# Performance work log

Measured on AMD Instinct MI355X. Metric: run time of the kernel, lower is better.

Reference implementation:

```python
import jax, jax.numpy as jnp
import numpy as np

B, S, H, A = 64, 2048, 512, 512


def setup_inputs() -> dict:
    key = jax.random.key(0)
    k1, k2, k3, k4, k5 = jax.random.split(key, 5)
    nn_outs = jax.random.normal(k1, (B, S, H), dtype=jnp.float32)
    # lengths in [1, S] so every row has at least one valid step
    batch_lens = jax.random.randint(k2, (B,), 1, S + 1, dtype=jnp.int64)
    # learned params: context vector ~ U(-0.1, 0.1), Linear(H -> A)
    context = jax.random.uniform(k3, (A,), dtype=jnp.float32, minval=-0.1, maxval=0.1)
    proj_w = jax.random.uniform(k4, (A, H), dtype=jnp.float32, minval=-0.1, maxval=0.1)
    proj_b = jax.random.uniform(k5, (A,), dtype=jnp.float32, minval=-0.1, maxval=0.1)
    return {"nn_outs": nn_outs, "batch_lens": batch_lens,
            "context": context, "proj_w": proj_w, "proj_b": proj_b}


def reference(nn_outs, batch_lens, context, proj_w, proj_b):
    # proj = tanh(Linear(nn_outs)): (B, S, A)
    proj = jnp.tanh(jnp.einsum('bsh,ah->bsa', nn_outs, proj_w) + proj_b)
    # attention scores: (B, S)
    scores = jnp.einsum('bsa,a->bs', proj, context)
    # variable-length masked softmax (replaces the per-batch python loop)
    mask = jnp.arange(nn_outs.shape[1])[None, :] < batch_lens[:, None]  # (B, S)
    scores = jnp.where(mask, scores, -jnp.inf)
    atten = jax.nn.softmax(scores, axis=-1)
    atten = jnp.where(mask, atten, 0.0)  # padded positions exactly zero
    # weighted sum over steps: (B, H)
    return jnp.einsum('bs,bsh->bh', atten, nn_outs)
```

## Files before the change

kernel.cpp:

```cpp
#include <hip/hip_runtime.h>

#define BB 64
#define SS 2048
#define HH 512
#define MROWS (BB*SS)

typedef __attribute__((ext_vector_type(8))) short short8;
typedef __attribute__((ext_vector_type(4))) float f32x4;

__device__ inline unsigned short f2bf(float f){
  unsigned int u = __float_as_uint(f);
  u += 0x7FFFu + ((u >> 16) & 1u);
  return (unsigned short)(u >> 16);
}

__device__ inline int read_len(const void* lens, int i){
  const int* p = (const int*)lens;
  if (p[1] == 0) return (int)((const long long*)lens)[i];
  return p[i];
}

__device__ inline float fast_tanh(float x){
  x = fminf(fmaxf(x, -15.f), 15.f);
  float e = __expf(2.f * x);
  return (e - 1.f) / (e + 1.f);
}

__device__ inline void gload16(const void* gptr, void* lptr){
  __builtin_amdgcn_global_load_lds(
      (const __attribute__((address_space(1))) void*)gptr,
      (__attribute__((address_space(3))) void*)lptr, 16, 0, 0);
}

__device__ inline short8 cvt8p(float4 x0, float4 x1){
  short8 r;
  r[0] = (short)f2bf(x0.x); r[1] = (short)f2bf(x0.y);
  r[2] = (short)f2bf(x0.z); r[3] = (short)f2bf(x0.w);
  r[4] = (short)f2bf(x1.x); r[5] = (short)f2bf(x1.y);
  r[6] = (short)f2bf(x1.z); r[7] = (short)f2bf(x1.w);
  return r;
}

__global__ __launch_bounds__(256) void convw_kernel(
    const float* __restrict__ W, unsigned short* __restrict__ Wb)
{
  size_t base = (size_t)blockIdx.x * 64 * HH;
  int t = threadIdx.x;
  #pragma unroll
  for (int j = 0; j < 32; j++) {
    size_t idx = base + (size_t)j * 1024 + t * 4;
    float4 v = *(const float4*)(W + idx);
    unsigned int p0 = (unsigned int)f2bf(v.x) | ((unsigned int)f2bf(v.y) << 16);
    unsigned int p1 = (unsigned int)f2bf(v.z) | ((unsigned int)f2bf(v.w) << 16);
    *(uint2*)(Wb + idx) = make_uint2(p0, p1);
  }
}

__global__ __launch_bounds__(512, 2) void scores_n512(
    const float* __restrict__ X, const unsigned short* __restrict__ Wb,
    const void* __restrict__ lens, const float* __restrict__ ctx,
    const float* __restrict__ pb, float* __restrict__ scr)
{
  int bid = blockIdx.x;
  int mtile = (bid & 7) * 128 + (bid >> 3);
  int s_start = (mtile * 128) & (SS - 1);
  int b = (mtile * 128) >> 11;
  if (s_start >= read_len(lens, b)) return;

  __shared__ __align__(16) unsigned short As[128 * 64];
  __shared__ __align__(16) unsigned short Bs[2][512 * 64];

  int tid = threadIdx.x;
  int lane = tid & 63;
  int w = tid >> 6;
  int wm = w >> 2, wn = w & 3;
  int l15 = lane & 15, g = lane >> 4;

  f32x4 acc[4][8];
  #pragma unroll
  for (int i = 0; i < 4; i++)
    #pragma unroll
    for (int j = 0; j < 8; j++) acc[i][j] = (f32x4)0.f;

  int arow = tid >> 2;
  int alg0 = (tid & 3) * 2;
  const float* Ag = X + (size_t)(mtile * 128 + arow) * HH + alg0 * 8;
  int apg0 = (alg0)     ^ (arow & 7);
  int apg1 = (alg0 + 1) ^ (arow & 7);

  int brow = lane >> 3;
  int blg = (lane & 7) ^ brow;
  const unsigned short* Bg = Wb + (size_t)brow * HH + blg * 8;

  float4 ar[4];

#define A_ISSUE(KT) { const float* p_ = Ag + (KT); \
    ar[0] = *(const float4*)p_;       ar[1] = *(const float4*)(p_ + 4); \
    ar[2] = *(const float4*)(p_ + 8); ar[3] = *(const float4*)(p_ + 12); }

#define A_WRITE() { \
    *(short8*)&As[arow * 64 + apg0 * 8] = cvt8p(ar[0], ar[1]); \
    *(short8*)&As[arow * 64 + apg1 * 8] = cvt8p(ar[2], ar[3]); }

#define B_ISSUE(BUF, KT) { _Pragma("unroll") for (int i_ = 0; i_ < 8; i_++) { \
    int j_ = w * 8 + i_; \
    gload16(Bg + (size_t)(j_ * 8) * HH + (KT), &Bs[BUF][(j_ * 8) * 64]); } }

  A_ISSUE(0)
  B_ISSUE(0, 0)
  A_WRITE()
  __syncthreads();

  int cur = 0;
  for (int t = 0; t < 8; ++t) {
    if (t < 7) {
      A_ISSUE((t + 1) * 64)
      B_ISSUE(cur ^ 1, (t + 1) * 64)
    }
    #pragma unroll
    for (int kk = 0; kk < 64; kk += 32) {
      int ga = g + (kk >> 3);
      int pga = (ga ^ (l15 & 7)) * 8;
      short8 af[4];
      #pragma unroll
      for (int im = 0; im < 4; im++) {
        int r = wm * 64 + im * 16 + l15;
        af[im] = *(const short8*)&As[r * 64 + pga];
      }
      #pragma unroll
      for (int in = 0; in < 8; in++) {
        int r2 = wn * 128 + in * 16 + l15;
        short8 bfr = *(const short8*)&Bs[cur][r2 * 64 + pga];
        #pragma unroll
        for (int im = 0; im < 4; im++)
          acc[im][in] = __builtin_amdgcn_mfma_f32_16x16x32_bf16(
              af[im], bfr, acc[im][in], 0, 0, 0);
      }
    }
    __syncthreads();
    if (t < 7) A_WRITE()
    __syncthreads();
    cur ^= 1;
  }

  float pbv[8], ctxv[8];
  #pragma unroll
  for (int in = 0; in < 8; in++) {
    int a_g = wn * 128 + in * 16 + l15;
    pbv[in] = pb[a_g];
    ctxv[in] = ctx[a_g];
  }
  float* red = (float*)As;
  #pragma unroll
  for (int im = 0; im < 4; im++) {
    #pragma unroll
    for (int r = 0; r < 4; r++) {
      float rowsum = 0.f;
      #pragma unroll
      for (int in = 0; in < 8; in++)
        rowsum += fast_tanh(acc[im][in][r] + pbv[in]) * ctxv[in];
      #pragma unroll
      for (int m = 1; m < 16; m <<= 1)
        rowsum += __shfl_xor(rowsum, m, 64);
      if (l15 == 0)
        red[wn * 128 + wm * 64 + im * 16 + g * 4 + r] = rowsum;
    }
  }
  __syncthreads();
  if (tid < 128) {
    float s = red[tid] + red[128 + tid] + red[256 + tid] + red[384 + tid];
    scr[(size_t)mtile * 128 + tid] = s;
  }
}

__global__ __launch_bounds__(256) void softmax_kernel(
    const float* __restrict__ scr, const void* __restrict__ lens,
    float* __restrict__ wts)
{
  int b = blockIdx.x;
  int tid = threadIdx.x;
  int len = read_len(lens, b);
  float sc[8];
  #pragma unroll
  for (int i = 0; i < 8; i++)
    sc[i] = scr[(size_t)b * SS + tid + i * 256];
  float m = -1e30f;
  #pragma unroll
  for (int i = 0; i < 8; i++)
    if (tid + i * 256 < len) m = fmaxf(m, sc[i]);
  #pragma unroll
  for (int off = 1; off < 64; off <<= 1) m = fmaxf(m, __shfl_xor(m, off, 64));
  __shared__ float redm[4];
  __shared__ float reds[4];
  int w = tid >> 6, lane = tid & 63;
  if (lane == 0) redm[w] = m;
  __syncthreads();
  m = fmaxf(fmaxf(redm[0], redm[1]), fmaxf(redm[2], redm[3]));
  float e[8]; float sum = 0.f;
  #pragma unroll
  for (int i = 0; i < 8; i++) {
    int s = tid + i * 256;
    e[i] = (s < len) ? __expf(sc[i] - m) : 0.f;
    sum += e[i];
  }
  #pragma unroll
  for (int off = 1; off < 64; off <<= 1) sum += __shfl_xor(sum, off, 64);
  if (lane == 0) reds[w] = sum;
  __syncthreads();
  sum = reds[0] + reds[1] + reds[2] + reds[3];
  float inv = 1.f / sum;
  #pragma unroll
  for (int i = 0; i < 8; i++) {
    int s = tid + i * 256;
    wts[(size_t)b * SS + s] = e[i] * inv;
  }
}

__global__ __launch_bounds__(256) void softmax8_kernel(
    const float* __restrict__ sp, const void* __restrict__ lens,
    float* __restrict__ wts)
{
  int b = blockIdx.x;
  int tid = threadIdx.x;
  int len = read_len(lens, b);
  float sc[8];
  #pragma unroll
  for (int i = 0; i < 8; i++) {
    int s = tid + i * 256;
    size_t row = (size_t)b * SS + s;
    float v = 0.f;
    #pragma unroll
    for (int p = 0; p < 8; p++) v += sp[(size_t)p * MROWS + row];
    sc[i] = v;
  }
  float m = -1e30f;
  #pragma unroll
  for (int i = 0; i < 8; i++)
    if (tid + i * 256 < len) m = fmaxf(m, sc[i]);
  #pragma unroll
  for (int off = 1; off < 64; off <<= 1) m = fmaxf(m, __shfl_xor(m, off, 64));
  __shared__ float redm[4];
  __shared__ float reds[4];
  int w = tid >> 6, lane = tid & 63;
  if (lane == 0) redm[w] = m;
  __syncthreads();
  m = fmaxf(fmaxf(redm[0], redm[1]), fmaxf(redm[2], redm[3]));
  float e[8]; float sum = 0.f;
  #pragma unroll
  for (int i = 0; i < 8; i++) {
    int s = tid + i * 256;
    e[i] = (s < len) ? __expf(sc[i] - m) : 0.f;
    sum += e[i];
  }
  #pragma unroll
  for (int off = 1; off < 64; off <<= 1) sum += __shfl_xor(sum, off, 64);
  if (lane == 0) reds[w] = sum;
  __syncthreads();
  sum = reds[0] + reds[1] + reds[2] + reds[3];
  float inv = 1.f / sum;
  #pragma unroll
  for (int i = 0; i < 8; i++) {
    int s = tid + i * 256;
    wts[(size_t)b * SS + s] = e[i] * inv;
  }
}

__global__ __launch_bounds__(256) void wsum_kernel(
    const float* __restrict__ X, const float* __restrict__ wts,
    const void* __restrict__ lens, float* __restrict__ op)
{
  int sc = blockIdx.x;
  int b  = blockIdx.y;
  int tid = threadIdx.x;
  int s0 = sc * 128;
  int len = read_len(lens, b);
  int cnt = min(128, len - s0);
  float* o = op + ((size_t)sc * BB + b) * HH;
  if (cnt <= 0) {
    *(float2*)(o + tid * 2) = make_float2(0.f, 0.f);
    return;
  }
  __shared__ float wsh[128];
  __shared__ f32x4 red[128];
  if (tid < 128) wsh[tid] = wts[(size_t)b * SS + s0 + tid];
  __syncthreads();
  int h = (tid & 127) * 4;
  int sr = tid >> 7;
  f32x4 acc = (f32x4)0.f;
  for (int i = sr; i < cnt; i += 2) {
    float wv = wsh[i];
    const float* xr = X + ((size_t)b * SS + s0 + i) * HH + h;
    float4 xv = *(const float4*)xr;
    acc[0] += wv * xv.x;
    acc[1] += wv * xv.y;
    acc[2] += wv * xv.z;
    acc[3] += wv * xv.w;
  }
  if (sr == 1) red[tid & 127] = acc;
  __syncthreads();
  if (sr == 0) {
    f32x4 r2 = red[tid];
    acc[0] += r2[0]; acc[1] += r2[1]; acc[2] += r2[2]; acc[3] += r2[3];
    *(f32x4*)(o + h) = acc;
  }
}

__global__ __launch_bounds__(512) void reduce_kernel(
    const float* __restrict__ op, float* __restrict__ out)
{
  int b = blockIdx.x;
  int h = threadIdx.x;
  float v = 0.f;
  #pragma unroll
  for (int sc = 0; sc < 16; sc++) v += op[((size_t)sc * BB + b) * HH + h];
  out[(size_t)b * HH + h] = v;
}

__global__ __launch_bounds__(256) void scores_fb(
    const float* __restrict__ X, const void* __restrict__ lens,
    const float* __restrict__ ctx, const float* __restrict__ W,
    const float* __restrict__ pb, float* __restrict__ sp)
{
  int bid = blockIdx.x;
  int wg = (bid & 7) * 512 + (bid >> 3);
  int ntile = wg & 3;
  int mtile = wg >> 2;
  int s_start = (mtile * 128) & (SS - 1);
  int b = (mtile * 128) >> 11;
  if (s_start >= read_len(lens, b)) return;

  __shared__ unsigned short As[128 * 72];
  __shared__ unsigned short Bs[128 * 72];

  int tid = threadIdx.x;
  int lane = tid & 63;
  int w = tid >> 6;
  int wm = w >> 1, wn = w & 1;
  int l15 = lane & 15, g = lane >> 4;

  f32x4 acc[4][4];
  #pragma unroll
  for (int i = 0; i < 4; i++)
    #pragma unroll
    for (int j = 0; j < 4; j++) acc[i][j] = (f32x4)0.f;

  int srow = tid >> 4;
  int scol = (tid & 15) * 4;
  const float* Xbase = X + (size_t)(mtile * 128) * HH;
  const float* Wbase = W + (size_t)(ntile * 128) * HH;

  for (int kt = 0; kt < HH; kt += 64) {
    #pragma unroll
    for (int i = 0; i < 8; i++) {
      int row = srow + i * 16;
      float4 va = *(const float4*)(Xbase + (size_t)row * HH + kt + scol);
      unsigned int p0 = (unsigned int)f2bf(va.x) | ((unsigned int)f2bf(va.y) << 16);
      unsigned int p1 = (unsigned int)f2bf(va.z) | ((unsigned int)f2bf(va.w) << 16);
      *(uint2*)&As[row * 72 + scol] = make_uint2(p0, p1);
      float4 vb = *(const float4*)(Wbase + (size_t)row * HH + kt + scol);
      unsigned int q0 = (unsigned int)f2bf(vb.x) | ((unsigned int)f2bf(vb.y) << 16);
      unsigned int q1 = (unsigned int)f2bf(vb.z) | ((unsigned int)f2bf(vb.w) << 16);
      *(uint2*)&Bs[row * 72 + scol] = make_uint2(q0, q1);
    }
    __syncthreads();
    #pragma unroll
    for (int kk = 0; kk < 64; kk += 32) {
      short8 af[4], bfr[4];
      int ko = kk + g * 8;
      #pragma unroll
      for (int im = 0; im < 4; im++)
        af[im] = *(const short8*)&As[(wm * 64 + im * 16 + l15) * 72 + ko];
      #pragma unroll
      for (int in = 0; in < 4; in++)
        bfr[in] = *(const short8*)&Bs[(wn * 64 + in * 16 + l15) * 72 + ko];
      #pragma unroll
      for (int im = 0; im < 4; im++)
        #pragma unroll
        for (int in = 0; in < 4; in++)
          acc[im][in] = __builtin_amdgcn_mfma_f32_16x16x32_bf16(
              af[im], bfr[in], acc[im][in], 0, 0, 0);
    }
    __syncthreads();
  }

  #pragma unroll
  for (int im = 0; im < 4; im++) {
    #pragma unroll
    for (int r = 0; r < 4; r++) {
      float rowsum = 0.f;
      #pragma unroll
      for (int in = 0; in < 4; in++) {
        int a_g = ntile * 128 + wn * 64 + in * 16 + l15;
        rowsum += fast_tanh(acc[im][in][r] + pb[a_g]) * ctx[a_g];
      }
      #pragma unroll
      for (int m = 1; m < 16; m <<= 1)
        rowsum += __shfl_xor(rowsum, m, 64);
      if (l15 == 0) {
        int rowg = mtile * 128 + wm * 64 + im * 16 + g * 4 + r;
        sp[(size_t)(ntile * 2 + wn) * MROWS + rowg] = rowsum;
      }
    }
  }
}

extern "C" void kernel_launch(void* const* d_in, const int* in_sizes, int n_in,
                              void* d_out, int out_size, void* d_ws, size_t ws_size,
                              hipStream_t stream) {
  const float* X   = (const float*)d_in[0];
  const void*  lens = d_in[1];
  const float* ctx = (const float*)d_in[2];
  const float* W   = (const float*)d_in[3];
  const float* pb  = (const float*)d_in[4];
  float* out = (float*)d_out;

  char* ws = (char*)d_ws;
  const size_t WB_BYTES = (size_t)HH * HH * 2;
  const size_t SC_BYTES = (size_t)MROWS * 4;
  const size_t WT_BYTES = (size_t)BB * SS * 4;
  const size_t OP_BYTES = 16ull * BB * HH * 4;
  const size_t NEED = WB_BYTES + SC_BYTES + WT_BYTES + OP_BYTES;

  if (ws_size >= NEED) {
    unsigned short* Wb = (unsigned short*)ws;
    float* scr = (float*)(ws + WB_BYTES);
    float* wts = (float*)(ws + WB_BYTES + SC_BYTES);
    float* op  = (float*)(ws + WB_BYTES + SC_BYTES + WT_BYTES);

    convw_kernel<<<8, 256, 0, stream>>>(W, Wb);
    scores_n512<<<1024, 512, 0, stream>>>(X, Wb, lens, ctx, pb, scr);
    softmax_kernel<<<BB, 256, 0, stream>>>(scr, lens, wts);
    wsum_kernel<<<dim3(16, BB), 256, 0, stream>>>(X, wts, lens, op);
    reduce_kernel<<<BB, 512, 0, stream>>>(op, out);
  } else {
    const size_t SP_BYTES = 8ull * MROWS * 4;
    float* sp  = (float*)ws;
    float* wts = (float*)(ws + SP_BYTES);
    float* op  = (float*)(ws + SP_BYTES + WT_BYTES);

    scores_fb<<<4096, 256, 0, stream>>>(X, lens, ctx, W, pb, sp);
    softmax8_kernel<<<BB, 256, 0, stream>>>(sp, lens, wts);
    wsum_kernel<<<dim3(16, BB), 256, 0, stream>>>(X, wts, lens, op);
    reduce_kernel<<<BB, 512, 0, stream>>>(op, out);
  }
}
```

Baseline: 131.4 us.

## Restructure scores GEMM to 1024-thread blocks with padded K=32 double buffers

The scores kernel is rewritten to use 16 waves per block (2x8 wave grid, 4x4 MFMA tiles per wave) instead of 8 waves with 4x8 tiles. The K step drops from 64 to 32, and both A and B are double-buffered in LDS using padded rows of stride 40 rather than XOR swizzling. B is now loaded through registers instead of direct global-to-LDS loads, and the blockIdx remapping is removed. Per-wave register pressure falls and the loop needs one barrier per iteration instead of two, at the cost of twice as many iterations and a different LDS bank-conflict pattern.

```diff
diff --git a/kernel.cpp b/kernel.cpp
--- a/kernel.cpp
+++ b/kernel.cpp
@@ -26,19 +26,10 @@
   return (e - 1.f) / (e + 1.f);
 }
 
-__device__ inline void gload16(const void* gptr, void* lptr){
-  __builtin_amdgcn_global_load_lds(
-      (const __attribute__((address_space(1))) void*)gptr,
-      (__attribute__((address_space(3))) void*)lptr, 16, 0, 0);
-}
-
-__device__ inline short8 cvt8p(float4 x0, float4 x1){
-  short8 r;
-  r[0] = (short)f2bf(x0.x); r[1] = (short)f2bf(x0.y);
-  r[2] = (short)f2bf(x0.z); r[3] = (short)f2bf(x0.w);
-  r[4] = (short)f2bf(x1.x); r[5] = (short)f2bf(x1.y);
-  r[6] = (short)f2bf(x1.z); r[7] = (short)f2bf(x1.w);
-  return r;
+__device__ inline uint2 cvt4p(float4 v){
+  unsigned int p0 = (unsigned int)f2bf(v.x) | ((unsigned int)f2bf(v.y) << 16);
+  unsigned int p1 = (unsigned int)f2bf(v.z) | ((unsigned int)f2bf(v.w) << 16);
+  return make_uint2(p0, p1);
 }
 
 __global__ __launch_bounds__(256) void convw_kernel(
@@ -50,103 +41,87 @@
   for (int j = 0; j < 32; j++) {
     size_t idx = base + (size_t)j * 1024 + t * 4;
     float4 v = *(const float4*)(W + idx);
-    unsigned int p0 = (unsigned int)f2bf(v.x) | ((unsigned int)f2bf(v.y) << 16);
-    unsigned int p1 = (unsigned int)f2bf(v.z) | ((unsigned int)f2bf(v.w) << 16);
-    *(uint2*)(Wb + idx) = make_uint2(p0, p1);
-  }
-}
-
-__global__ __launch_bounds__(512, 2) void scores_n512(
+    *(uint2*)(Wb + idx) = cvt4p(v);
+  }
+}
+
+__global__ __launch_bounds__(1024) void scores_v10(
     const float* __restrict__ X, const unsigned short* __restrict__ Wb,
     const void* __restrict__ lens, const float* __restrict__ ctx,
     const float* __restrict__ pb, float* __restrict__ scr)
 {
-  int bid = blockIdx.x;
-  int mtile = (bid & 7) * 128 + (bid >> 3);
+  int mtile = blockIdx.x;
   int s_start = (mtile * 128) & (SS - 1);
   int b = (mtile * 128) >> 11;
   if (s_start >= read_len(lens, b)) return;
 
-  __shared__ __align__(16) unsigned short As[128 * 64];
-  __shared__ __align__(16) unsigned short Bs[2][512 * 64];
+  __shared__ __align__(16) unsigned short As[2][128 * 40];
+  __shared__ __align__(16) unsigned short Bs[2][512 * 40];
 
   int tid = threadIdx.x;
   int lane = tid & 63;
   int w = tid >> 6;
-  int wm = w >> 2, wn = w & 3;
+  int wm = w >> 3, wn = w & 7;
   int l15 = lane & 15, g = lane >> 4;
 
-  f32x4 acc[4][8];
+  f32x4 acc[4][4];
   #pragma unroll
   for (int i = 0; i < 4; i++)
     #pragma unroll
-    for (int j = 0; j < 8; j++) acc[i][j] = (f32x4)0.f;
-
-  int arow = tid >> 2;
-  int alg0 = (tid & 3) * 2;
-  const float* Ag = X + (size_t)(mtile * 128 + arow) * HH + alg0 * 8;
-  int apg0 = (alg0)     ^ (arow & 7);
-  int apg1 = (alg0 + 1) ^ (arow & 7);
-
-  int brow = lane >> 3;
-  int blg = (lane & 7) ^ brow;
-  const unsigned short* Bg = Wb + (size_t)brow * HH + blg * 8;
-
-  float4 ar[4];
-
-#define A_ISSUE(KT) { const float* p_ = Ag + (KT); \
-    ar[0] = *(const float4*)p_;       ar[1] = *(const float4*)(p_ + 4); \
-    ar[2] = *(const float4*)(p_ + 8); ar[3] = *(const float4*)(p_ + 12); }
-
-#define A_WRITE() { \
-    *(short8*)&As[arow * 64 + apg0 * 8] = cvt8p(ar[0], ar[1]); \
-    *(short8*)&As[arow * 64 + apg1 * 8] = cvt8p(ar[2], ar[3]); }
-
-#define B_ISSUE(BUF, KT) { _Pragma("unroll") for (int i_ = 0; i_ < 8; i_++) { \
-    int j_ = w * 8 + i_; \
-    gload16(Bg + (size_t)(j_ * 8) * HH + (KT), &Bs[BUF][(j_ * 8) * 64]); } }
-
-  A_ISSUE(0)
-  B_ISSUE(0, 0)
-  A_WRITE()
+    for (int j = 0; j < 4; j++) acc[i][j] = (f32x4)0.f;
+
+  int arow = tid >> 3;
+  int acg  = tid & 7;
+  const float* Ag = X + (size_t)(mtile * 128 + arow) * HH + acg * 4;
+
+  int brow = tid >> 1;
+  int bh   = tid & 1;
+  const unsigned short* Bg = Wb + (size_t)brow * HH + bh * 16;
+
+  float4 av;
+  short8 bv0, bv1;
+
+#define ISSUE(KT) { \
+    av  = *(const float4*)(Ag + (KT)); \
+    bv0 = *(const short8*)(Bg + (KT)); \
+    bv1 = *(const short8*)(Bg + (KT) + 8); }
+
+#define WRITE(BUF) { \
+    *(uint2*)&As[BUF][arow * 40 + acg * 4] = cvt4p(av); \
+    *(short8*)&Bs[BUF][brow * 40 + bh * 16]     = bv0; \
+    *(short8*)&Bs[BUF][brow * 40 + bh * 16 + 8] = bv1; }
+
+  ISSUE(0)
+  WRITE(0)
   __syncthreads();
 
   int cur = 0;
-  for (int t = 0; t < 8; ++t) {
-    if (t < 7) {
-      A_ISSUE((t + 1) * 64)
-      B_ISSUE(cur ^ 1, (t + 1) * 64)
-    }
-    #pragma unroll
-    for (int kk = 0; kk < 64; kk += 32) {
-      int ga = g + (kk >> 3);
-      int pga = (ga ^ (l15 & 7)) * 8;
-      short8 af[4];
-      #pragma unroll
-      for (int im = 0; im < 4; im++) {
-        int r = wm * 64 + im * 16 + l15;
-        af[im] = *(const short8*)&As[r * 64 + pga];
-      }
-      #pragma unroll
-      for (int in = 0; in < 8; in++) {
-        int r2 = wn * 128 + in * 16 + l15;
-        short8 bfr = *(const short8*)&Bs[cur][r2 * 64 + pga];
-        #pragma unroll
-        for (int im = 0; im < 4; im++)
-          acc[im][in] = __builtin_amdgcn_mfma_f32_16x16x32_bf16(
-              af[im], bfr, acc[im][in], 0, 0, 0);
-      }
-    }
-    __syncthreads();
-    if (t < 7) A_WRITE()
+  for (int t = 0; t < 16; ++t) {
+    if (t < 15) ISSUE((t + 1) * 32)
+    short8 af[4];
+    #pragma unroll
+    for (int im = 0; im < 4; im++) {
+      int r = wm * 64 + im * 16 + l15;
+      af[im] = *(const short8*)&As[cur][r * 40 + g * 8];
+    }
+    #pragma unroll
+    for (int in = 0; in < 4; in++) {
+      int r2 = wn * 64 + in * 16 + l15;
+      short8 bfr = *(const short8*)&Bs[cur][r2 * 40 + g * 8];
+      #pragma unroll
+      for (int im = 0; im < 4; im++)
+        acc[im][in] = __builtin_amdgcn_mfma_f32_16x16x32_bf16(
+            af[im], bfr, acc[im][in], 0, 0, 0);
+    }
+    if (t < 15) WRITE(cur ^ 1)
     __syncthreads();
     cur ^= 1;
   }
 
-  float pbv[8], ctxv[8];
-  #pragma unroll
-  for (int in = 0; in < 8; in++) {
-    int a_g = wn * 128 + in * 16 + l15;
+  float pbv[4], ctxv[4];
+  #pragma unroll
+  for (int in = 0; in < 4; in++) {
+    int a_g = wn * 64 + in * 16 + l15;
     pbv[in] = pb[a_g];
     ctxv[in] = ctx[a_g];
   }
@@ -157,18 +132,22 @@
     for (int r = 0; r < 4; r++) {
       float rowsum = 0.f;
       #pragma unroll
-      for (int in = 0; in < 8; in++)
+      for (int in = 0; in < 4; in++)
         rowsum += fast_tanh(acc[im][in][r] + pbv[in]) * ctxv[in];
       #pragma unroll
       for (int m = 1; m < 16; m <<= 1)
         rowsum += __shfl_xor(rowsum, m, 64);
-      if (l15 == 0)
-        red[wn * 128 + wm * 64 + im * 16 + g * 4 + r] = rowsum;
+      if (l15 == 0) {
+        int rowg = wm * 64 + im * 16 + g * 4 + r;
+        red[wn * 128 + rowg] = rowsum;
+      }
     }
   }
   __syncthreads();
   if (tid < 128) {
-    float s = red[tid] + red[128 + tid] + red[256 + tid] + red[384 + tid];
+    float s = 0.f;
+    #pragma unroll
+    for (int q = 0; q < 8; q++) s += red[q * 128 + tid];
     scr[(size_t)mtile * 128 + tid] = s;
   }
 }
@@ -184,55 +163,6 @@
   #pragma unroll
   for (int i = 0; i < 8; i++)
     sc[i] = scr[(size_t)b * SS + tid + i * 256];
-  float m = -1e30f;
-  #pragma unroll
-  for (int i = 0; i < 8; i++)
-    if (tid + i * 256 < len) m = fmaxf(m, sc[i]);
-  #pragma unroll
-  for (int off = 1; off < 64; off <<= 1) m = fmaxf(m, __shfl_xor(m, off, 64));
-  __shared__ float redm[4];
-  __shared__ float reds[4];
-  int w = tid >> 6, lane = tid & 63;
-  if (lane == 0) redm[w] = m;
-  __syncthreads();
-  m = fmaxf(fmaxf(redm[0], redm[1]), fmaxf(redm[2], redm[3]));
-  float e[8]; float sum = 0.f;
-  #pragma unroll
-  for (int i = 0; i < 8; i++) {
-    int s = tid + i * 256;
-    e[i] = (s < len) ? __expf(sc[i] - m) : 0.f;
-    sum += e[i];
-  }
-  #pragma unroll
-  for (int off = 1; off < 64; off <<= 1) sum += __shfl_xor(sum, off, 64);
-  if (lane == 0) reds[w] = sum;
-  __syncthreads();
-  sum = reds[0] + reds[1] + reds[2] + reds[3];
-  float inv = 1.f / sum;
-  #pragma unroll
-  for (int i = 0; i < 8; i++) {
-    int s = tid + i * 256;
-    wts[(size_t)b * SS + s] = e[i] * inv;
-  }
-}
-
-__global__ __launch_bounds__(256) void softmax8_kernel(
-    const float* __restrict__ sp, const void* __restrict__ lens,
-    float* __restrict__ wts)
-{
-  int b = blockIdx.x;
-  int tid = threadIdx.x;
-  int len = read_len(lens, b);
-  float sc[8];
-  #pragma unroll
-  for (int i = 0; i < 8; i++) {
-    int s = tid + i * 256;
-    size_t row = (size_t)b * SS + s;
-    float v = 0.f;
-    #pragma unroll
-    for (int p = 0; p < 8; p++) v += sp[(size_t)p * MROWS + row];
-    sc[i] = v;
-  }
   float m = -1e30f;
   #pragma unroll
   for (int i = 0; i < 8; i++)
@@ -354,13 +284,9 @@
     for (int i = 0; i < 8; i++) {
       int row = srow + i * 16;
       float4 va = *(const float4*)(Xbase + (size_t)row * HH + kt + scol);
-      unsigned int p0 = (unsigned int)f2bf(va.x) | ((unsigned int)f2bf(va.y) << 16);
-      unsigned int p1 = (unsigned int)f2bf(va.z) | ((unsigned int)f2bf(va.w) << 16);
-      *(uint2*)&As[row * 72 + scol] = make_uint2(p0, p1);
+      *(uint2*)&As[row * 72 + scol] = cvt4p(va);
       float4 vb = *(const float4*)(Wbase + (size_t)row * HH + kt + scol);
-      unsigned int q0 = (unsigned int)f2bf(vb.x) | ((unsigned int)f2bf(vb.y) << 16);
-      unsigned int q1 = (unsigned int)f2bf(vb.z) | ((unsigned int)f2bf(vb.w) << 16);
-      *(uint2*)&Bs[row * 72 + scol] = make_uint2(q0, q1);
+      *(uint2*)&Bs[row * 72 + scol] = cvt4p(vb);
     }
     __syncthreads();
     #pragma unroll
@@ -401,6 +327,55 @@
         sp[(size_t)(ntile * 2 + wn) * MROWS + rowg] = rowsum;
       }
     }
+  }
+}
+
+__global__ __launch_bounds__(256) void softmax8_kernel(
+    const float* __restrict__ sp, const void* __restrict__ lens,
+    float* __restrict__ wts)
+{
+  int b = blockIdx.x;
+  int tid = threadIdx.x;
+  int len = read_len(lens, b);
+  float sc[8];
+  #pragma unroll
+  for (int i = 0; i < 8; i++) {
+    int s = tid + i * 256;
+    size_t row = (size_t)b * SS + s;
+    float v = 0.f;
+    #pragma unroll
+    for (int p = 0; p < 8; p++) v += sp[(size_t)p * MROWS + row];
+    sc[i] = v;
+  }
+  float m = -1e30f;
+  #pragma unroll
+  for (int i = 0; i < 8; i++)
+    if (tid + i * 256 < len) m = fmaxf(m, sc[i]);
+  #pragma unroll
+  for (int off = 1; off < 64; off <<= 1) m = fmaxf(m, __shfl_xor(m, off, 64));
+  __shared__ float redm[4];
+  __shared__ float reds[4];
+  int w = tid >> 6, lane = tid & 63;
+  if (lane == 0) redm[w] = m;
+  __syncthreads();
+  m = fmaxf(fmaxf(redm[0], redm[1]), fmaxf(redm[2], redm[3]));
+  float e[8]; float sum = 0.f;
+  #pragma unroll
+  for (int i = 0; i < 8; i++) {
+    int s = tid + i * 256;
+    e[i] = (s < len) ? __expf(sc[i] - m) : 0.f;
+    sum += e[i];
+  }
+  #pragma unroll
+  for (int off = 1; off < 64; off <<= 1) sum += __shfl_xor(sum, off, 64);
+  if (lane == 0) reds[w] = sum;
+  __syncthreads();
+  sum = reds[0] + reds[1] + reds[2] + reds[3];
+  float inv = 1.f / sum;
+  #pragma unroll
+  for (int i = 0; i < 8; i++) {
+    int s = tid + i * 256;
+    wts[(size_t)b * SS + s] = e[i] * inv;
   }
 }
 
@@ -428,7 +403,7 @@
     float* op  = (float*)(ws + WB_BYTES + SC_BYTES + WT_BYTES);
 
     convw_kernel<<<8, 256, 0, stream>>>(W, Wb);
-    scores_n512<<<1024, 512, 0, stream>>>(X, Wb, lens, ctx, pb, scr);
+    scores_v10<<<1024, 1024, 0, stream>>>(X, Wb, lens, ctx, pb, scr);
     softmax_kernel<<<BB, 256, 0, stream>>>(scr, lens, wts);
     wsum_kernel<<<dim3(16, BB), 256, 0, stream>>>(X, wts, lens, op);
     reduce_kernel<<<BB, 512, 0, stream>>>(op, out);
```

Measured after the change: 172.1 us. 1.31x slower.

## Double-buffer A tile in scores GEMM and fuse softmax into weighted-sum kernel

Applied to the files above, without the earlier changes.

The scores GEMM now double-buffers the bf16 A tile in shared memory, which removes one __syncthreads per k-step. Shared memory per block grows by 16 KB, which may affect occupancy at 2 blocks per CU. The separate softmax kernel is removed: each weighted-sum block recomputes the per-batch max and sum from the raw scores, then normalizes its own 128-step chunk. This drops one launch and the weights buffer round-trip, but every one of the 16 chunk blocks redundantly reads the full 2048-score row.

```diff
diff --git a/kernel.cpp b/kernel.cpp
--- a/kernel.cpp
+++ b/kernel.cpp
@@ -56,7 +56,7 @@
   }
 }
 
-__global__ __launch_bounds__(512, 2) void scores_n512(
+__global__ __launch_bounds__(512, 2) void scores_v11(
     const float* __restrict__ X, const unsigned short* __restrict__ Wb,
     const void* __restrict__ lens, const float* __restrict__ ctx,
     const float* __restrict__ pb, float* __restrict__ scr)
@@ -67,7 +67,7 @@
   int b = (mtile * 128) >> 11;
   if (s_start >= read_len(lens, b)) return;
 
-  __shared__ __align__(16) unsigned short As[128 * 64];
+  __shared__ __align__(16) unsigned short As[2][128 * 64];
   __shared__ __align__(16) unsigned short Bs[2][512 * 64];
 
   int tid = threadIdx.x;
@@ -98,9 +98,9 @@
     ar[0] = *(const float4*)p_;       ar[1] = *(const float4*)(p_ + 4); \
     ar[2] = *(const float4*)(p_ + 8); ar[3] = *(const float4*)(p_ + 12); }
 
-#define A_WRITE() { \
-    *(short8*)&As[arow * 64 + apg0 * 8] = cvt8p(ar[0], ar[1]); \
-    *(short8*)&As[arow * 64 + apg1 * 8] = cvt8p(ar[2], ar[3]); }
+#define A_WRITE(BUF) { \
+    *(short8*)&As[BUF][arow * 64 + apg0 * 8] = cvt8p(ar[0], ar[1]); \
+    *(short8*)&As[BUF][arow * 64 + apg1 * 8] = cvt8p(ar[2], ar[3]); }
 
 #define B_ISSUE(BUF, KT) { _Pragma("unroll") for (int i_ = 0; i_ < 8; i_++) { \
     int j_ = w * 8 + i_; \
@@ -108,7 +108,7 @@
 
   A_ISSUE(0)
   B_ISSUE(0, 0)
-  A_WRITE()
+  A_WRITE(0)
   __syncthreads();
 
   int cur = 0;
@@ -125,7 +125,7 @@
       #pragma unroll
       for (int im = 0; im < 4; im++) {
         int r = wm * 64 + im * 16 + l15;
-        af[im] = *(const short8*)&As[r * 64 + pga];
+        af[im] = *(const short8*)&As[cur][r * 64 + pga];
       }
       #pragma unroll
       for (int in = 0; in < 8; in++) {
@@ -137,8 +137,7 @@
               af[im], bfr, acc[im][in], 0, 0, 0);
       }
     }
-    __syncthreads();
-    if (t < 7) A_WRITE()
+    if (t < 7) A_WRITE(cur ^ 1)
     __syncthreads();
     cur ^= 1;
   }
@@ -173,8 +172,180 @@
   }
 }
 
-__global__ __launch_bounds__(256) void softmax_kernel(
-    const float* __restrict__ scr, const void* __restrict__ lens,
+__global__ __launch_bounds__(256) void wsum2_kernel(
+    const float* __restrict__ X, const float* __restrict__ scr,
+    const void* __restrict__ lens, float* __restrict__ op)
+{
+  int sc = blockIdx.x;
+  int b  = blockIdx.y;
+  int tid = threadIdx.x;
+  int s0 = sc * 128;
+  int len = read_len(lens, b);
+  int cnt = min(128, len - s0);
+  float* o = op + ((size_t)sc * BB + b) * HH;
+  if (cnt <= 0) {
+    *(float2*)(o + tid * 2) = make_float2(0.f, 0.f);
+    return;
+  }
+
+  __shared__ float redm[4], reds[4];
+  __shared__ float wsh[128];
+  __shared__ f32x4 red[128];
+
+  int wv = tid >> 6, lane = tid & 63;
+  float scv[8];
+  float m = -1e30f;
+  #pragma unroll
+  for (int i = 0; i < 8; i++) {
+    int s = tid + i * 256;
+    scv[i] = scr[(size_t)b * SS + s];
+    if (s < len) m = fmaxf(m, scv[i]);
+  }
+  #pragma unroll
+  for (int off = 1; off < 64; off <<= 1) m = fmaxf(m, __shfl_xor(m, off, 64));
+  if (lane == 0) redm[wv] = m;
+  __syncthreads();
+  m = fmaxf(fmaxf(redm[0], redm[1]), fmaxf(redm[2], redm[3]));
+  float sum = 0.f;
+  #pragma unroll
+  for (int i = 0; i < 8; i++) {
+    int s = tid + i * 256;
+    sum += (s < len) ? __expf(scv[i] - m) : 0.f;
+  }
+  #pragma unroll
+  for (int off = 1; off < 64; off <<= 1) sum += __shfl_xor(sum, off, 64);
+  if (lane == 0) reds[wv] = sum;
+  __syncthreads();
+  float inv = 1.f / (reds[0] + reds[1] + reds[2] + reds[3]);
+
+  if (tid < 128) {
+    int s = s0 + tid;
+    wsh[tid] = (s < len) ? __expf(scr[(size_t)b * SS + s] - m) * inv : 0.f;
+  }
+  __syncthreads();
+
+  int h = (tid & 127) * 4;
+  int sr = tid >> 7;
+  f32x4 acc = (f32x4)0.f;
+  for (int i = sr; i < cnt; i += 2) {
+    float wvv = wsh[i];
+    const float* xr = X + ((size_t)b * SS + s0 + i) * HH + h;
+    float4 xv = *(const float4*)xr;
+    acc[0] += wvv * xv.x;
+    acc[1] += wvv * xv.y;
+    acc[2] += wvv * xv.z;
+    acc[3] += wvv * xv.w;
+  }
+  if (sr == 1) red[tid & 127] = acc;
+  __syncthreads();
+  if (sr == 0) {
+    f32x4 r2 = red[tid];
+    acc[0] += r2[0]; acc[1] += r2[1]; acc[2] += r2[2]; acc[3] += r2[3];
+    *(f32x4*)(o + h) = acc;
+  }
+}
+
+__global__ __launch_bounds__(512) void reduce_kernel(
+    const float* __restrict__ op, float* __restrict__ out)
+{
+  int b = blockIdx.x;
+  int h = threadIdx.x;
+  float v = 0.f;
+  #pragma unroll
+  for (int sc = 0; sc < 16; sc++) v += op[((size_t)sc * BB + b) * HH + h];
+  out[(size_t)b * HH + h] = v;
+}
+
+__global__ __launch_bounds__(256) void scores_fb(
+    const float* __restrict__ X, const void* __restrict__ lens,
+    const float* __restrict__ ctx, const float* __restrict__ W,
+    const float* __restrict__ pb, float* __restrict__ sp)
+{
+  int bid = blockIdx.x;
+  int wg = (bid & 7) * 512 + (bid >> 3);
+  int ntile = wg & 3;
+  int mtile = wg >> 2;
+  int s_start = (mtile * 128) & (SS - 1);
+  int b = (mtile * 128) >> 11;
+  if (s_start >= read_len(lens, b)) return;
+
+  __shared__ unsigned short As[128 * 72];
+  __shared__ unsigned short Bs[128 * 72];
+
+  int tid = threadIdx.x;
+  int lane = tid & 63;
+  int w = tid >> 6;
+  int wm = w >> 1, wn = w & 1;
+  int l15 = lane & 15, g = lane >> 4;
+
+  f32x4 acc[4][4];
+  #pragma unroll
+  for (int i = 0; i < 4; i++)
+    #pragma unroll
+    for (int j = 0; j < 4; j++) acc[i][j] = (f32x4)0.f;
+
+  int srow = tid >> 4;
+  int scol = (tid & 15) * 4;
+  const float* Xbase = X + (size_t)(mtile * 128) * HH;
+  const float* Wbase = W + (size_t)(ntile * 128) * HH;
+
+  for (int kt = 0; kt < HH; kt += 64) {
+    #pragma unroll
+    for (int i = 0; i < 8; i++) {
+      int row = srow + i * 16;
+      float4 va = *(const float4*)(Xbase + (size_t)row * HH + kt + scol);
+      unsigned int p0 = (unsigned int)f2bf(va.x) | ((unsigned int)f2bf(va.y) << 16);
+      unsigned int p1 = (unsigned int)f2bf(va.z) | ((unsigned int)f2bf(va.w) << 16);
+      *(uint2*)&As[row * 72 + scol] = make_uint2(p0, p1);
+      float4 vb = *(const float4*)(Wbase + (size_t)row * HH + kt + scol);
+      unsigned int q0 = (unsigned int)f2bf(vb.x) | ((unsigned int)f2bf(vb.y) << 16);
+      unsigned int q1 = (unsigned int)f2bf(vb.z) | ((unsigned int)f2bf(vb.w) << 16);
+      *(uint2*)&Bs[row * 72 + scol] = make_uint2(q0, q1);
+    }
+    __syncthreads();
+    #pragma unroll
+    for (int kk = 0; kk < 64; kk += 32) {
+      short8 af[4], bfr[4];
+      int ko = kk + g * 8;
+      #pragma unroll
+      for (int im = 0; im < 4; im++)
+        af[im] = *(const short8*)&As[(wm * 64 + im * 16 + l15) * 72 + ko];
+      #pragma unroll
+      for (int in = 0; in < 4; in++)
+        bfr[in] = *(const short8*)&Bs[(wn * 64 + in * 16 + l15) * 72 + ko];
+      #pragma unroll
+      for (int im = 0; im < 4; im++)
+        #pragma unroll
+        for (int in = 0; in < 4; in++)
+          acc[im][in] = __builtin_amdgcn_mfma_f32_16x16x32_bf16(
+              af[im], bfr[in], acc[im][in], 0, 0, 0);
+    }
+    __syncthreads();
+  }
+
+  #pragma unroll
+  for (int im = 0; im < 4; im++) {
+    #pragma unroll
+    for (int r = 0; r < 4; r++) {
+      float rowsum = 0.f;
+      #pragma unroll
+      for (int in = 0; in < 4; in++) {
+        int a_g = ntile * 128 + wn * 64 + in * 16 + l15;
+        rowsum += fast_tanh(acc[im][in][r] + pb[a_g]) * ctx[a_g];
+      }
+      #pragma unroll
+      for (int m = 1; m < 16; m <<= 1)
+        rowsum += __shfl_xor(rowsum, m, 64);
+      if (l15 == 0) {
+        int rowg = mtile * 128 + wm * 64 + im * 16 + g * 4 + r;
+        sp[(size_t)(ntile * 2 + wn) * MROWS + rowg] = rowsum;
+      }
+    }
+  }
+}
+
+__global__ __launch_bounds__(256) void softmax8_kernel(
+    const float* __restrict__ sp, const void* __restrict__ lens,
     float* __restrict__ wts)
 {
   int b = blockIdx.x;
@@ -182,8 +353,14 @@
   int len = read_len(lens, b);
   float sc[8];
   #pragma unroll
-  for (int i = 0; i < 8; i++)
-    sc[i] = scr[(size_t)b * SS + tid + i * 256];
+  for (int i = 0; i < 8; i++) {
+    int s = tid + i * 256;
+    size_t row = (size_t)b * SS + s;
+    float v = 0.f;
+    #pragma unroll
+    for (int p = 0; p < 8; p++) v += sp[(size_t)p * MROWS + row];
+    sc[i] = v;
+  }
   float m = -1e30f;
   #pragma unroll
   for (int i = 0; i < 8; i++)
@@ -216,56 +393,7 @@
   }
 }
 
-__global__ __launch_bounds__(256) void softmax8_kernel(
-    const float* __restrict__ sp, const void* __restrict__ lens,
-    float* __restrict__ wts)
-{
-  int b = blockIdx.x;
-  int tid = threadIdx.x;
-  int len = read_len(lens, b);
-  float sc[8];
-  #pragma unroll
-  for (int i = 0; i < 8; i++) {
-    int s = tid + i * 256;
-    size_t row = (size_t)b * SS + s;
-    float v = 0.f;
-    #pragma unroll
-    for (int p = 0; p < 8; p++) v += sp[(size_t)p * MROWS + row];
-    sc[i] = v;
-  }
-  float m = -1e30f;
-  #pragma unroll
-  for (int i = 0; i < 8; i++)
-    if (tid + i * 256 < len) m = fmaxf(m, sc[i]);
-  #pragma unroll
-  for (int off = 1; off < 64; off <<= 1) m = fmaxf(m, __shfl_xor(m, off, 64));
-  __shared__ float redm[4];
-  __shared__ float reds[4];
-  int w = tid >> 6, lane = tid & 63;
-  if (lane == 0) redm[w] = m;
-  __syncthreads();
-  m = fmaxf(fmaxf(redm[0], redm[1]), fmaxf(redm[2], redm[3]));
-  float e[8]; float sum = 0.f;
-  #pragma unroll
-  for (int i = 0; i < 8; i++) {
-    int s = tid + i * 256;
-    e[i] = (s < len) ? __expf(sc[i] - m) : 0.f;
-    sum += e[i];
-  }
-  #pragma unroll
-  for (int off = 1; off < 64; off <<= 1) sum += __shfl_xor(sum, off, 64);
-  if (lane == 0) reds[w] = sum;
-  __syncthreads();
-  sum = reds[0] + reds[1] + reds[2] + reds[3];
-  float inv = 1.f / sum;
-  #pragma unroll
-  for (int i = 0; i < 8; i++) {
-    int s = tid + i * 256;
-    wts[(size_t)b * SS + s] = e[i] * inv;
-  }
-}
-
-__global__ __launch_bounds__(256) void wsum_kernel(
+__global__ __launch_bounds__(256) void wsum_fb(
     const float* __restrict__ X, const float* __restrict__ wts,
     const void* __restrict__ lens, float* __restrict__ op)
 {
@@ -305,105 +433,6 @@
   }
 }
 
-__global__ __launch_bounds__(512) void reduce_kernel(
-    const float* __restrict__ op, float* __restrict__ out)
-{
-  int b = blockIdx.x;
-  int h = threadIdx.x;
-  float v = 0.f;
-  #pragma unroll
-  for (int sc = 0; sc < 16; sc++) v += op[((size_t)sc * BB + b) * HH + h];
-  out[(size_t)b * HH + h] = v;
-}
-
-__global__ __launch_bounds__(256) void scores_fb(
-    const float* __restrict__ X, const void* __restrict__ lens,
-    const float* __restrict__ ctx, const float* __restrict__ W,
-    const float* __restrict__ pb, float* __restrict__ sp)
-{
-  int bid = blockIdx.x;
-  int wg = (bid & 7) * 512 + (bid >> 3);
-  int ntile = wg & 3;
-  int mtile = wg >> 2;
-  int s_start = (mtile * 128) & (SS - 1);
-  int b = (mtile * 128) >> 11;
-  if (s_start >= read_len(lens, b)) return;
-
-  __shared__ unsigned short As[128 * 72];
-  __shared__ unsigned short Bs[128 * 72];
-
-  int tid = threadIdx.x;
-  int lane = tid & 63;
-  int w = tid >> 6;
-  int wm = w >> 1, wn = w & 1;
-  int l15 = lane & 15, g = lane >> 4;
-
-  f32x4 acc[4][4];
-  #pragma unroll
-  for (int i = 0; i < 4; i++)
-    #pragma unroll
-    for (int j = 0; j < 4; j++) acc[i][j] = (f32x4)0.f;
-
-  int srow = tid >> 4;
-  int scol = (tid & 15) * 4;
-  const float* Xbase = X + (size_t)(mtile * 128) * HH;
-  const float* Wbase = W + (size_t)(ntile * 128) * HH;
-
-  for (int kt = 0; kt < HH; kt += 64) {
-    #pragma unroll
-    for (int i = 0; i < 8; i++) {
-      int row = srow + i * 16;
-      float4 va = *(const float4*)(Xbase + (size_t)row * HH + kt + scol);
-      unsigned int p0 = (unsigned int)f2bf(va.x) | ((unsigned int)f2bf(va.y) << 16);
-      unsigned int p1 = (unsigned int)f2bf(va.z) | ((unsigned int)f2bf(va.w) << 16);
-      *(uint2*)&As[row * 72 + scol] = make_uint2(p0, p1);
-      float4 vb = *(const float4*)(Wbase + (size_t)row * HH + kt + scol);
-      unsigned int q0 = (unsigned int)f2bf(vb.x) | ((unsigned int)f2bf(vb.y) << 16);
-      unsigned int q1 = (unsigned int)f2bf(vb.z) | ((unsigned int)f2bf(vb.w) << 16);
-      *(uint2*)&Bs[row * 72 + scol] = make_uint2(q0, q1);
-    }
-    __syncthreads();
-    #pragma unroll
-    for (int kk = 0; kk < 64; kk += 32) {
-      short8 af[4], bfr[4];
-      int ko = kk + g * 8;
-      #pragma unroll
-      for (int im = 0; im < 4; im++)
-        af[im] = *(const short8*)&As[(wm * 64 + im * 16 + l15) * 72 + ko];
-      #pragma unroll
-      for (int in = 0; in < 4; in++)
-        bfr[in] = *(const short8*)&Bs[(wn * 64 + in * 16 + l15) * 72 + ko];
-      #pragma unroll
-      for (int im = 0; im < 4; im++)
-        #pragma unroll
-        for (int in = 0; in < 4; in++)
-          acc[im][in] = __builtin_amdgcn_mfma_f32_16x16x32_bf16(
-              af[im], bfr[in], acc[im][in], 0, 0, 0);
-    }
-    __syncthreads();
-  }
-
-  #pragma unroll
-  for (int im = 0; im < 4; im++) {
-    #pragma unroll
-    for (int r = 0; r < 4; r++) {
-      float rowsum = 0.f;
-      #pragma unroll
-      for (int in = 0; in < 4; in++) {
-        int a_g = ntile * 128 + wn * 64 + in * 16 + l15;
-        rowsum += fast_tanh(acc[im][in][r] + pb[a_g]) * ctx[a_g];
-      }
-      #pragma unroll
-      for (int m = 1; m < 16; m <<= 1)
-        rowsum += __shfl_xor(rowsum, m, 64);
-      if (l15 == 0) {
-        int rowg = mtile * 128 + wm * 64 + im * 16 + g * 4 + r;
-        sp[(size_t)(ntile * 2 + wn) * MROWS + rowg] = rowsum;
-      }
-    }
-  }
-}
-
 extern "C" void kernel_launch(void* const* d_in, const int* in_sizes, int n_in,
                               void* d_out, int out_size, void* d_ws, size_t ws_size,
                               hipStream_t stream) {
@@ -417,30 +446,28 @@
   char* ws = (char*)d_ws;
   const size_t WB_BYTES = (size_t)HH * HH * 2;
   const size_t SC_BYTES = (size_t)MROWS * 4;
-  const size_t WT_BYTES = (size_t)BB * SS * 4;
   const size_t OP_BYTES = 16ull * BB * HH * 4;
-  const size_t NEED = WB_BYTES + SC_BYTES + WT_BYTES + OP_BYTES;
+  const size_t NEED = WB_BYTES + SC_BYTES + OP_BYTES;
 
   if (ws_size >= NEED) {
     unsigned short* Wb = (unsigned short*)ws;
     float* scr = (float*)(ws + WB_BYTES);
-    float* wts = (float*)(ws + WB_BYTES + SC_BYTES);
-    float* op  = (float*)(ws + WB_BYTES + SC_BYTES + WT_BYTES);
+    float* op  = (float*)(ws + WB_BYTES + SC_BYTES);
 
     convw_kernel<<<8, 256, 0, stream>>>(W, Wb);
-    scores_n512<<<1024, 512, 0, stream>>>(X, Wb, lens, ctx, pb, scr);
-    softmax_kernel<<<BB, 256, 0, stream>>>(scr, lens, wts);
-    wsum_kernel<<<dim3(16, BB), 256, 0, stream>>>(X, wts, lens, op);
+    scores_v11<<<1024, 512, 0, stream>>>(X, Wb, lens, ctx, pb, scr);
+    wsum2_kernel<<<dim3(16, BB), 256, 0, stream>>>(X, scr, lens, op);
     reduce_kernel<<<BB, 512, 0, stream>>>(op, out);
   } else {
     const size_t SP_BYTES = 8ull * MROWS * 4;
+    const size_t WT_BYTES = (size_t)BB * SS * 4;
     float* sp  = (float*)ws;
     float* wts = (float*)(ws + SP_BYTES);
     float* op  = (float*)(ws + SP_BYTES + WT_BYTES);
 
     scores_fb<<<4096, 256, 0, stream>>>(X, lens, ctx, W, pb, sp);
     softmax8_kernel<<<BB, 256, 0, stream>>>(sp, lens, wts);
-    wsum_kernel<<<dim3(16, BB), 256, 0, stream>>>(X, wts, lens, op);
+    wsum_fb<<<dim3(16, BB), 256, 0, stream>>>(X, wts, lens, op);
     reduce_kernel<<<BB, 512, 0, stream>>>(op, out);
   }
 }
```

New measurement: 133.2 us. No clear change (+1.4%).
